# Kernel optimization log

Hardware: AMD Instinct MI355X
Metric: run time of the kernel (lower is better)

Reference implementation:

```python
import jax, jax.numpy as jnp
import numpy as np

N_NODES = 100000
N_EDGES = 1200000
NFEAT = 64
NHID = 64
NCLASS = 16
BN_EPS = 1e-5
L2_EPS = 1e-12


def setup_inputs() -> dict:
    key = jax.random.key(0)
    ks = jax.random.split(key, 8)
    edge_index = jax.random.randint(ks[0], (2, N_EDGES), 0, N_NODES, dtype=jnp.int64)
    x = jax.random.normal(ks[1], (N_NODES, NFEAT), dtype=jnp.float32)
    # SAGEConv params: lin_l (neighbor path, has bias), lin_r (root path, no bias)
    W_l = jax.random.normal(ks[2], (NHID, NFEAT), dtype=jnp.float32) * (1.0 / np.sqrt(NFEAT))
    b_l = jnp.zeros((NHID,), dtype=jnp.float32)
    W_r = jax.random.normal(ks[3], (NHID, NFEAT), dtype=jnp.float32) * (1.0 / np.sqrt(NFEAT))
    # BatchNorm1d affine params
    gamma = jnp.ones((NHID,), dtype=jnp.float32)
    beta = jnp.zeros((NHID,), dtype=jnp.float32)
    # final fc (xavier-ish scale, zero bias per weights_init)
    W_fc = jax.random.normal(ks[4], (NCLASS, NHID), dtype=jnp.float32) * (1.0 / np.sqrt(NHID))
    b_fc = jnp.zeros((NCLASS,), dtype=jnp.float32)
    return {"edge_index": edge_index, "x": x, "W_l": W_l, "b_l": b_l,
            "W_r": W_r, "gamma": gamma, "beta": beta, "W_fc": W_fc, "b_fc": b_fc}


def reference(edge_index, x, W_l, b_l, W_r, gamma, beta, W_fc, b_fc):
    N = x.shape[0]
    src, dst = edge_index[0], edge_index[1]
    # SAGEConv mean aggregation: gather x at source nodes, scatter-mean to dst
    msgs = x[src]                                                  # [E, F]
    sums = jax.ops.segment_sum(msgs, dst, num_segments=N)         # [N, F]
    cnt = jax.ops.segment_sum(jnp.ones((src.shape[0], 1), x.dtype), dst, num_segments=N)
    mean = sums / jnp.maximum(cnt, 1.0)
    # out = lin_l(mean_neighbors) + lin_r(x_root)
    h = mean @ W_l.T + b_l + x @ W_r.T                              # [N, H]
    # normalize=True -> L2 normalize rows (F.normalize semantics)
    h = h / jnp.maximum(jnp.linalg.norm(h, axis=-1, keepdims=True), L2_EPS)
    # transition: ReLU -> BatchNorm1d (training stats) -> Dropout (identity in eval)
    h = jax.nn.relu(h)
    mu = jnp.mean(h, axis=0)
    var = jnp.var(h, axis=0)
    h = (h - mu) / jnp.sqrt(var + BN_EPS) * gamma + beta
    return h @ W_fc.T + b_fc                                        # [N, C]
```

## Files before the change

kernel.cpp:

```cpp
#include <hip/hip_runtime.h>
#include <hip/hip_bf16.h>


typedef __attribute__((ext_vector_type(8))) short short8;
typedef __attribute__((ext_vector_type(4))) float f32x4;

__device__ __forceinline__ unsigned short f2bf(float f) {
    unsigned int u = __builtin_bit_cast(unsigned int, f);
    u += 0x7FFFu + ((u >> 16) & 1u);
    return (unsigned short)(u >> 16);
}
__device__ __forceinline__ float bf2f(unsigned short s) {
    return __builtin_bit_cast(float, ((unsigned int)s) << 16);
}

#define CHUNK 8192

__global__ __launch_bounds__(256) void k_prep(const int* __restrict__ eidx,
                                              int* __restrict__ cnt,
                                              const float4* __restrict__ x4,
                                              ushort4* __restrict__ xbf,
                                              int E, int NB, int NBLK,
                                              int n4, int do_x) {
    __shared__ int lh[256];
    const int tid = threadIdx.x;
    if ((int)blockIdx.x < NBLK) {
        lh[tid] = 0;
        __syncthreads();
        const int base = blockIdx.x * CHUNK;
        for (int i = tid; i < CHUNK; i += 256) {
            int e = base + i;
            if (e < E) atomicAdd(&lh[eidx[E + e] >> 9], 1);
        }
        __syncthreads();
        if (tid < NB) cnt[(size_t)tid * NBLK + blockIdx.x] = lh[tid];
    } else if (do_x) {
        int t = ((int)blockIdx.x - NBLK) * 256 + tid;
        if (t < n4) {
            float4 v = x4[t];
            xbf[t] = make_ushort4(f2bf(v.x), f2bf(v.y), f2bf(v.z), f2bf(v.w));
        }
    }
}

__global__ __launch_bounds__(256) void k_scanbkt(int* __restrict__ cnt,
                                                 int* __restrict__ btot,
                                                 int NBLK) {
    __shared__ int swv[4];
    const int b = blockIdx.x;
    const int t = threadIdx.x;
    int v = (t < NBLK) ? cnt[(size_t)b * NBLK + t] : 0;
    const int lane = t & 63, wid = t >> 6;
    int s = v;
#pragma unroll
    for (int off = 1; off < 64; off <<= 1) {
        int tt = __shfl_up(s, off);
        if (lane >= off) s += tt;
    }
    if (lane == 63) swv[wid] = s;
    __syncthreads();
    if (t == 0) {
        int a = 0;
#pragma unroll
        for (int w = 0; w < 4; ++w) { int tt = swv[w]; swv[w] = a; a += tt; }
    }
    __syncthreads();
    int excl = s - v + swv[wid];
    if (t < NBLK) cnt[(size_t)b * NBLK + t] = excl;
    if (t == 255) btot[b] = swv[3] + s;
}

__global__ __launch_bounds__(256) void k_bscanB(const int* __restrict__ btot,
                                                int* __restrict__ bbase,
                                                int* __restrict__ rowptr,
                                                int NB, int N, int E) {
    __shared__ int swv[4];
    const int t = threadIdx.x;
    int v = (t < NB) ? btot[t] : 0;
    const int lane = t & 63, wid = t >> 6;
    int s = v;
#pragma unroll
    for (int off = 1; off < 64; off <<= 1) {
        int tt = __shfl_up(s, off);
        if (lane >= off) s += tt;
    }
    if (lane == 63) swv[wid] = s;
    __syncthreads();
    if (t == 0) {
        int a = 0;
#pragma unroll
        for (int w = 0; w < 4; ++w) { int tt = swv[w]; swv[w] = a; a += tt; }
    }
    __syncthreads();
    if (t < NB) bbase[t] = s - v + swv[wid];
    if (t == 0) { bbase[NB] = E; rowptr[N] = E; }
}

__global__ __launch_bounds__(256) void k_bscatter(const int* __restrict__ eidx,
                                                  const int* __restrict__ cnt,
                                                  const int* __restrict__ bbase,
                                                  unsigned int* __restrict__ ebuf,
                                                  int E, int NB, int NBLK) {
    __shared__ int cur[256];
    const int tid = threadIdx.x;
    if (tid < NB)
        cur[tid] = bbase[tid] + cnt[(size_t)tid * NBLK + blockIdx.x];
    __syncthreads();
    const int base = blockIdx.x * CHUNK;
    for (int i = tid; i < CHUNK; i += 256) {
        int e = base + i;
        if (e < E) {
            int d = eidx[E + e];
            int s = eidx[e];
            int p = atomicAdd(&cur[d >> 9], 1);
            ebuf[p] = (unsigned int)s | ((unsigned int)(d & 511) << 17);
        }
    }
}

__global__ __launch_bounds__(256) void k_bfinal(const unsigned int* __restrict__ ebuf,
                                                const int* __restrict__ bbase,
                                                int* __restrict__ rowptr,
                                                int* __restrict__ colv, int N) {
    __shared__ int h[512];
    __shared__ int swv[4];
    const int b = blockIdx.x;
    const int tid = threadIdx.x;
    h[2 * tid] = 0;
    h[2 * tid + 1] = 0;
    __syncthreads();
    const int segb = bbase[b], sege = bbase[b + 1];
    for (int i = segb + tid; i < sege; i += 256)
        atomicAdd(&h[ebuf[i] >> 17], 1);
    __syncthreads();
    int a0 = h[2 * tid], a1 = h[2 * tid + 1];
    int ts = a0 + a1;
    const int lane = tid & 63, wid = tid >> 6;
    int s = ts;
#pragma unroll
    for (int off = 1; off < 64; off <<= 1) {
        int tt = __shfl_up(s, off);
        if (lane >= off) s += tt;
    }
    if (lane == 63) swv[wid] = s;
    __syncthreads();
    if (tid == 0) {
        int a = 0;
#pragma unroll
        for (int w = 0; w < 4; ++w) { int tt = swv[w]; swv[w] = a; a += tt; }
    }
    __syncthreads();
    int excl = s - ts + swv[wid];
    h[2 * tid] = excl;
    h[2 * tid + 1] = excl + a0;
    int node = b * 512 + 2 * tid;
    if (node < N) rowptr[node] = segb + excl;
    if (node + 1 < N) rowptr[node + 1] = segb + excl + a0;
    __syncthreads();
    for (int i = segb + tid; i < sege; i += 256) {
        unsigned int u = ebuf[i];
        int p = atomicAdd(&h[u >> 17], 1);
        colv[segb + p] = (int)(u & 0x1FFFFu);
    }
}

__global__ __launch_bounds__(256) void k_gather_bf(
        const uint2* __restrict__ xbf2, const int* __restrict__ rowptr,
        const int* __restrict__ colv, uint2* __restrict__ mh2, int N) {
    int t = blockIdx.x * 256 + threadIdx.x;
    int n = t >> 4;
    int l = t & 15;
    if (n >= N) return;
    int b = rowptr[n], e = rowptr[n + 1];
    float a0 = 0.f, a1 = 0.f, a2 = 0.f, a3 = 0.f;
    int p = b;
    for (; p + 4 <= e; p += 4) {
        int s0 = colv[p], s1 = colv[p + 1], s2 = colv[p + 2], s3 = colv[p + 3];
        uint2 v0 = xbf2[(size_t)s0 * 16 + l];
        uint2 v1 = xbf2[(size_t)s1 * 16 + l];
        uint2 v2 = xbf2[(size_t)s2 * 16 + l];
        uint2 v3 = xbf2[(size_t)s3 * 16 + l];
        a0 += bf2f((unsigned short)(v0.x & 0xFFFF)) + bf2f((unsigned short)(v1.x & 0xFFFF)) +
              bf2f((unsigned short)(v2.x & 0xFFFF)) + bf2f((unsigned short)(v3.x & 0xFFFF));
        a1 += bf2f((unsigned short)(v0.x >> 16)) + bf2f((unsigned short)(v1.x >> 16)) +
              bf2f((unsigned short)(v2.x >> 16)) + bf2f((unsigned short)(v3.x >> 16));
        a2 += bf2f((unsigned short)(v0.y & 0xFFFF)) + bf2f((unsigned short)(v1.y & 0xFFFF)) +
              bf2f((unsigned short)(v2.y & 0xFFFF)) + bf2f((unsigned short)(v3.y & 0xFFFF));
        a3 += bf2f((unsigned short)(v0.y >> 16)) + bf2f((unsigned short)(v1.y >> 16)) +
              bf2f((unsigned short)(v2.y >> 16)) + bf2f((unsigned short)(v3.y >> 16));
    }
    for (; p < e; ++p) {
        int s0 = colv[p];
        uint2 v0 = xbf2[(size_t)s0 * 16 + l];
        a0 += bf2f((unsigned short)(v0.x & 0xFFFF));
        a1 += bf2f((unsigned short)(v0.x >> 16));
        a2 += bf2f((unsigned short)(v0.y & 0xFFFF));
        a3 += bf2f((unsigned short)(v0.y >> 16));
    }
    float inv = 1.0f / fmaxf((float)(e - b), 1.0f);
    uint2 o;
    o.x = (unsigned int)f2bf(a0 * inv) | ((unsigned int)f2bf(a1 * inv) << 16);
    o.y = (unsigned int)f2bf(a2 * inv) | ((unsigned int)f2bf(a3 * inv) << 16);
    mh2[(size_t)n * 16 + l] = o;
}

__global__ __launch_bounds__(256) void k_gather_f32(
        const float4* __restrict__ x4, const int* __restrict__ rowptr,
        const int* __restrict__ colv, ushort4* __restrict__ mh, int N) {
    int t = blockIdx.x * 256 + threadIdx.x;
    int n = t >> 4;
    int l = t & 15;
    if (n >= N) return;
    int b = rowptr[n], e = rowptr[n + 1];
    float ax = 0.f, ay = 0.f, az = 0.f, aw = 0.f;
    int p = b;
    for (; p + 4 <= e; p += 4) {
        int s0 = colv[p], s1 = colv[p + 1], s2 = colv[p + 2], s3 = colv[p + 3];
        float4 v0 = x4[(size_t)s0 * 16 + l];
        float4 v1 = x4[(size_t)s1 * 16 + l];
        float4 v2 = x4[(size_t)s2 * 16 + l];
        float4 v3 = x4[(size_t)s3 * 16 + l];
        ax += (v0.x + v1.x) + (v2.x + v3.x);
        ay += (v0.y + v1.y) + (v2.y + v3.y);
        az += (v0.z + v1.z) + (v2.z + v3.z);
        aw += (v0.w + v1.w) + (v2.w + v3.w);
    }
    for (; p < e; ++p) {
        int s0 = colv[p];
        float4 v0 = x4[(size_t)s0 * 16 + l];
        ax += v0.x; ay += v0.y; az += v0.z; aw += v0.w;
    }
    float inv = 1.0f / fmaxf((float)(e - b), 1.0f);
    mh[(size_t)n * 16 + l] = make_ushort4(f2bf(ax * inv), f2bf(ay * inv),
                                          f2bf(az * inv), f2bf(aw * inv));
}

__global__ __launch_bounds__(256) void k_fused(
        const float* __restrict__ x,
        const unsigned short* __restrict__ xbf, int use_bf,
        const float* __restrict__ Wl, const float* __restrict__ bl,
        const float* __restrict__ Wr,
        unsigned short* __restrict__ mh,
        float* __restrict__ pstats, int N) {
    __shared__ float sRed[4][128];

    const int tid = threadIdx.x;
    const int wid = tid >> 6;
    const int lane = tid & 63;
    const int l15 = lane & 15;
    const int quad = lane >> 4;

    short8 bfrag[4][4];
#pragma unroll
    for (int c = 0; c < 4; ++c) {
#pragma unroll
        for (int f = 0; f < 4; ++f) {
            const int n = f * 16 + l15;
            const float* wsrc = (c < 2)
                ? (Wl + (size_t)n * 64 + c * 32 + quad * 8)
                : (Wr + (size_t)n * 64 + (c - 2) * 32 + quad * 8);
            float4 w0 = *(const float4*)wsrc;
            float4 w1 = *(const float4*)(wsrc + 4);
            union { short8 v; unsigned short u[8]; } pk;
            pk.u[0] = f2bf(w0.x); pk.u[1] = f2bf(w0.y);
            pk.u[2] = f2bf(w0.z); pk.u[3] = f2bf(w0.w);
            pk.u[4] = f2bf(w1.x); pk.u[5] = f2bf(w1.y);
            pk.u[6] = f2bf(w1.z); pk.u[7] = f2bf(w1.w);
            bfrag[c][f] = pk.v;
        }
    }

    float blv[4];
#pragma unroll
    for (int f = 0; f < 4; ++f) blv[f] = bl[f * 16 + l15];

    float psum[4] = {0.f, 0.f, 0.f, 0.f};
    float psq[4] = {0.f, 0.f, 0.f, 0.f};

    for (int t4 = 0; t4 < 4; ++t4) {
        const int tbase = blockIdx.x * 256 + wid * 64 + t4 * 16;
        const int mrow = tbase + l15;
        const int mld = (mrow < N) ? mrow : (N - 1);
        f32x4 acc[4] = {{0.f, 0.f, 0.f, 0.f}, {0.f, 0.f, 0.f, 0.f},
                        {0.f, 0.f, 0.f, 0.f}, {0.f, 0.f, 0.f, 0.f}};
#pragma unroll
        for (int c = 0; c < 2; ++c) {
            short8 a = *(const short8*)(mh + (size_t)mld * 64 + c * 32 + quad * 8);
#pragma unroll
            for (int f = 0; f < 4; ++f)
                acc[f] = __builtin_amdgcn_mfma_f32_16x16x32_bf16(a, bfrag[c][f], acc[f], 0, 0, 0);
        }
        if (use_bf) {
#pragma unroll
            for (int c = 0; c < 2; ++c) {
                short8 a = *(const short8*)(xbf + (size_t)mld * 64 + c * 32 + quad * 8);
#pragma unroll
                for (int f = 0; f < 4; ++f)
                    acc[f] = __builtin_amdgcn_mfma_f32_16x16x32_bf16(a, bfrag[c + 2][f], acc[f], 0, 0, 0);
            }
        } else {
#pragma unroll
            for (int c = 0; c < 2; ++c) {
                const float* xp = x + (size_t)mld * 64 + c * 32 + quad * 8;
                float4 a0 = *(const float4*)xp;
                float4 a1 = *(const float4*)(xp + 4);
                union { short8 v; unsigned short u[8]; } pk;
                pk.u[0] = f2bf(a0.x); pk.u[1] = f2bf(a0.y);
                pk.u[2] = f2bf(a0.z); pk.u[3] = f2bf(a0.w);
                pk.u[4] = f2bf(a1.x); pk.u[5] = f2bf(a1.y);
                pk.u[6] = f2bf(a1.z); pk.u[7] = f2bf(a1.w);
#pragma unroll
                for (int f = 0; f < 4; ++f)
                    acc[f] = __builtin_amdgcn_mfma_f32_16x16x32_bf16(pk.v, bfrag[c + 2][f], acc[f], 0, 0, 0);
            }
        }

#pragma unroll
        for (int reg = 0; reg < 4; ++reg) {
            const int node = tbase + quad * 4 + reg;
            float hv[4];
            float ss = 0.f;
#pragma unroll
            for (int f = 0; f < 4; ++f) {
                hv[f] = acc[f][reg] + blv[f];
                ss += hv[f] * hv[f];
            }
            ss += __shfl_xor(ss, 1);
            ss += __shfl_xor(ss, 2);
            ss += __shfl_xor(ss, 4);
            ss += __shfl_xor(ss, 8);
            float sc = 1.0f / fmaxf(sqrtf(ss), 1e-12f);
            if (node < N) {
#pragma unroll
                for (int f = 0; f < 4; ++f) {
                    float r = fmaxf(hv[f] * sc, 0.f);
                    unsigned short rb = f2bf(r);
                    float e = bf2f(rb);
                    mh[(size_t)node * 64 + f * 16 + l15] = rb;
                    psum[f] += e;
                    psq[f] += e * e;
                }
            }
        }
    }

#pragma unroll
    for (int f = 0; f < 4; ++f) {
        psum[f] += __shfl_xor(psum[f], 16);
        psum[f] += __shfl_xor(psum[f], 32);
        psq[f] += __shfl_xor(psq[f], 16);
        psq[f] += __shfl_xor(psq[f], 32);
    }
    if (lane < 16) {
#pragma unroll
        for (int f = 0; f < 4; ++f) {
            sRed[wid][f * 16 + l15] = psum[f];
            sRed[wid][64 + f * 16 + l15] = psq[f];
        }
    }
    __syncthreads();
    if (tid < 128) {
        float v = sRed[0][tid] + sRed[1][tid] + sRed[2][tid] + sRed[3][tid];
        pstats[(size_t)blockIdx.x * 128 + tid] = v;
    }
}

__global__ __launch_bounds__(64) void k_stats(const float* __restrict__ pstats,
                                              float* __restrict__ stats, int nblk) {
    int col = blockIdx.x;
    int l = threadIdx.x;
    float s = 0.f;
    for (int r = l; r < nblk; r += 64) s += pstats[(size_t)r * 128 + col];
    s += __shfl_xor(s, 1);
    s += __shfl_xor(s, 2);
    s += __shfl_xor(s, 4);
    s += __shfl_xor(s, 8);
    s += __shfl_xor(s, 16);
    s += __shfl_xor(s, 32);
    if (l == 0) stats[col] = s;
}

__global__ __launch_bounds__(256) void k_out(
        const unsigned short* __restrict__ h, const float* __restrict__ stats,
        const float* __restrict__ gamma, const float* __restrict__ beta,
        const float* __restrict__ Wfc, const float* __restrict__ bfc,
        float* __restrict__ out, int N) {
    __shared__ float sWm[64 * 16];
    __shared__ float sShift[64];
    __shared__ float sBase[16];
    const int tid = threadIdx.x;
    const float invN = 1.0f / (float)N;
    if (tid < 64) {
        float mu = stats[tid] * invN;
        float var = stats[64 + tid] * invN - mu * mu;
        float sc = gamma[tid] / sqrtf(var + 1e-5f);
        sShift[tid] = beta[tid] - mu * sc;
#pragma unroll
        for (int c = 0; c < 16; ++c) sWm[tid * 16 + c] = Wfc[c * 64 + tid] * sc;
    }
    __syncthreads();
    if (tid < 16) {
        float b = bfc[tid];
#pragma unroll
        for (int j = 0; j < 64; ++j) b += sShift[j] * Wfc[tid * 64 + j];
        sBase[tid] = b;
    }
    __syncthreads();
    int g = blockIdx.x * 256 + tid;
    int n = g >> 4;
    int c = g & 15;
    if (n >= N) return;
    const ushort4* h4 = (const ushort4*)(h + (size_t)n * 64);
    float acc = sBase[c];
#pragma unroll
    for (int jq = 0; jq < 16; ++jq) {
        ushort4 v = h4[jq];
        acc += bf2f(v.x) * sWm[(jq * 4 + 0) * 16 + c];
        acc += bf2f(v.y) * sWm[(jq * 4 + 1) * 16 + c];
        acc += bf2f(v.z) * sWm[(jq * 4 + 2) * 16 + c];
        acc += bf2f(v.w) * sWm[(jq * 4 + 3) * 16 + c];
    }
    out[(size_t)n * 16 + c] = acc;
}

extern "C" void kernel_launch(void* const* d_in, const int* in_sizes, int n_in,
                              void* d_out, int out_size, void* d_ws, size_t ws_size,
                              hipStream_t stream) {
    const int* eidx = (const int*)d_in[0];
    const float* x = (const float*)d_in[1];
    const float* Wl = (const float*)d_in[2];
    const float* bl = (const float*)d_in[3];
    const float* Wr = (const float*)d_in[4];
    const float* gamma = (const float*)d_in[5];
    const float* beta = (const float*)d_in[6];
    const float* Wfc = (const float*)d_in[7];
    const float* bfc = (const float*)d_in[8];
    float* out = (float*)d_out;

    const int E = in_sizes[0] / 2;
    const int N = in_sizes[1] / 64;
    const int NB = (N + 511) >> 9;
    const int NBLK = (E + CHUNK - 1) / CHUNK;
    const int fb2 = (N + 255) / 256;
    const int n4 = N * 16;

    int* cnt = (int*)d_ws;
    int* btot = cnt + (size_t)NB * NBLK;
    int* bbase = btot + NB;
    int* rowptr = bbase + NB + 1;
    float* pstats = (float*)(rowptr + N + 1);
    float* stats = pstats + (size_t)fb2 * 128;
    int* colv = (int*)(stats + 128);
    unsigned int* ebuf = (unsigned int*)(colv + E);
    unsigned short* mh = (unsigned short*)(ebuf + E);
    unsigned short* xbf = mh + (size_t)N * 64;

    size_t need_bf = (size_t)((char*)(xbf + (size_t)N * 64) - (char*)d_ws);
    const int use_bf = (ws_size >= need_bf) ? 1 : 0;

    int cbl = use_bf ? (n4 + 255) / 256 : 0;
    k_prep<<<NBLK + cbl, 256, 0, stream>>>(eidx, cnt, (const float4*)x,
                                           (ushort4*)xbf, E, NB, NBLK, n4, use_bf);
    k_scanbkt<<<NB, 256, 0, stream>>>(cnt, btot, NBLK);
    k_bscanB<<<1, 256, 0, stream>>>(btot, bbase, rowptr, NB, N, E);
    k_bscatter<<<NBLK, 256, 0, stream>>>(eidx, cnt, bbase, ebuf, E, NB, NBLK);
    k_bfinal<<<NB, 256, 0, stream>>>(ebuf, bbase, rowptr, colv, N);

    int gblocks = (int)(((size_t)N * 16 + 255) / 256);
    if (use_bf) {
        k_gather_bf<<<gblocks, 256, 0, stream>>>((const uint2*)xbf, rowptr, colv,
                                                 (uint2*)mh, N);
    } else {
        k_gather_f32<<<gblocks, 256, 0, stream>>>((const float4*)x, rowptr, colv,
                                                  (ushort4*)mh, N);
    }

    k_fused<<<fb2, 256, 0, stream>>>(x, xbf, use_bf, Wl, bl, Wr, mh, pstats, N);
    k_stats<<<128, 64, 0, stream>>>(pstats, stats, fb2);

    int oblocks = (int)(((size_t)N * 16 + 255) / 256);
    k_out<<<oblocks, 256, 0, stream>>>(mh, stats, gamma, beta, Wfc, bfc, out, N);
}
```

Measured before the change: 212.0 us.

## Merge CSR build and tail stages into cooperative kernels with grid sync

Replaces the five CSR-construction launches (histogram, per-bucket scan, bucket-base scan, scatter, per-bucket final sort) with one cooperative kernel that uses grid.sync between phases and recomputes the small bucket scan redundantly per block. It also fuses the linear/normalize/stats kernel, the stats reduction and the output projection into one cooperative kernel, with each block reducing the partial stats itself. The aim is to remove launch gaps and intermediate kernel boundaries, at the cost of grid-wide barriers and a grid capped by occupancy, so the bf16 cast loop now strides over fewer blocks. Both paths fall back to the old launches when the device does not support cooperative launch or occupancy is insufficient.

```diff
diff --git a/kernel.cpp b/kernel.cpp
--- a/kernel.cpp
+++ b/kernel.cpp
@@ -1,5 +1,8 @@
 #include <hip/hip_runtime.h>
 #include <hip/hip_bf16.h>
+#include <hip/hip_cooperative_groups.h>
+
+namespace cg = cooperative_groups;
 
 
 typedef __attribute__((ext_vector_type(8))) short short8;
@@ -15,6 +18,135 @@
 }
 
 #define CHUNK 8192
+
+__device__ __forceinline__ int exclScan256(int v, int* swv) {
+    const int t = threadIdx.x, lane = t & 63, wid = t >> 6;
+    __syncthreads();
+    int s = v;
+#pragma unroll
+    for (int off = 1; off < 64; off <<= 1) {
+        int tt = __shfl_up(s, off);
+        if (lane >= off) s += tt;
+    }
+    if (lane == 63) swv[wid] = s;
+    __syncthreads();
+    if (t == 0) {
+        int a = 0;
+#pragma unroll
+        for (int w = 0; w < 4; ++w) { int tt = swv[w]; swv[w] = a; a += tt; }
+    }
+    __syncthreads();
+    return s - v + swv[wid];
+}
+
+__global__ __launch_bounds__(256) void k_csr(
+        const int* __restrict__ eidx, int* __restrict__ cnt,
+        int* __restrict__ btot,
+        const float4* __restrict__ x4, ushort4* __restrict__ xbf,
+        unsigned int* __restrict__ ebuf,
+        int* __restrict__ rowptr, int* __restrict__ colv,
+        int E, int N, int NB, int NBLK, int n4, int do_x) {
+    cg::grid_group grid = cg::this_grid();
+    __shared__ int sh[512];
+    __shared__ int sb[257];
+    __shared__ int swv[4];
+    const int tid = threadIdx.x;
+    const int bid = blockIdx.x;
+    const int GD = gridDim.x;
+
+    if (bid < NBLK) {
+        sh[tid] = 0;
+        __syncthreads();
+        const int base = bid * CHUNK;
+        for (int i = tid; i < CHUNK; i += 256) {
+            int e = base + i;
+            if (e < E) atomicAdd(&sh[eidx[E + e] >> 9], 1);
+        }
+        __syncthreads();
+        if (tid < NB) cnt[(size_t)tid * NBLK + bid] = sh[tid];
+    } else if (do_x) {
+        const int ncast = GD - NBLK;
+        for (int i = (bid - NBLK) * 256 + tid; i < n4; i += ncast * 256) {
+            float4 v = x4[i];
+            xbf[i] = make_ushort4(f2bf(v.x), f2bf(v.y), f2bf(v.z), f2bf(v.w));
+        }
+    }
+    __threadfence();
+    grid.sync();
+
+    if (bid < NB) {
+        int v = (tid < NBLK) ? cnt[(size_t)bid * NBLK + tid] : 0;
+        int excl = exclScan256(v, swv);
+        if (tid < NBLK) cnt[(size_t)bid * NBLK + tid] = excl;
+        if (tid == 255) btot[bid] = excl + v;
+    }
+    __threadfence();
+    grid.sync();
+
+    if (bid < NBLK) {
+        int bv = (tid < NB) ? btot[tid] : 0;
+        int bexcl = exclScan256(bv, swv);
+        sh[tid] = (tid < NB) ? (bexcl + cnt[(size_t)tid * NBLK + bid]) : 0;
+        __syncthreads();
+        const int base = bid * CHUNK;
+        for (int i = tid; i < CHUNK; i += 256) {
+            int e = base + i;
+            if (e < E) {
+                int d = eidx[E + e];
+                int s = eidx[e];
+                int p = atomicAdd(&sh[d >> 9], 1);
+                ebuf[p] = (unsigned int)s | ((unsigned int)(d & 511) << 17);
+            }
+        }
+    }
+    __threadfence();
+    grid.sync();
+
+    if (bid < NB) {
+        int bv = (tid < NB) ? btot[tid] : 0;
+        int bexcl = exclScan256(bv, swv);
+        sb[tid] = bexcl;
+        __syncthreads();
+        const int segb = sb[bid];
+        const int sege = segb + btot[bid];
+        sh[2 * tid] = 0;
+        sh[2 * tid + 1] = 0;
+        __syncthreads();
+        for (int i = segb + tid; i < sege; i += 256)
+            atomicAdd(&sh[ebuf[i] >> 17], 1);
+        __syncthreads();
+        int a0 = sh[2 * tid], a1 = sh[2 * tid + 1];
+        int ts = a0 + a1;
+        const int lane = tid & 63, wid = tid >> 6;
+        int s = ts;
+#pragma unroll
+        for (int off = 1; off < 64; off <<= 1) {
+            int tt = __shfl_up(s, off);
+            if (lane >= off) s += tt;
+        }
+        if (lane == 63) swv[wid] = s;
+        __syncthreads();
+        if (tid == 0) {
+            int a = 0;
+#pragma unroll
+            for (int w = 0; w < 4; ++w) { int tt = swv[w]; swv[w] = a; a += tt; }
+        }
+        __syncthreads();
+        int excl = s - ts + swv[wid];
+        sh[2 * tid] = excl;
+        sh[2 * tid + 1] = excl + a0;
+        int node = bid * 512 + 2 * tid;
+        if (node < N) rowptr[node] = segb + excl;
+        if (node + 1 < N) rowptr[node + 1] = segb + excl + a0;
+        __syncthreads();
+        for (int i = segb + tid; i < sege; i += 256) {
+            unsigned int u = ebuf[i];
+            int p = atomicAdd(&sh[u >> 17], 1);
+            colv[segb + p] = (int)(u & 0x1FFFFu);
+        }
+        if (bid == 0 && tid == 0) rowptr[N] = E;
+    }
+}
 
 __global__ __launch_bounds__(256) void k_prep(const int* __restrict__ eidx,
                                               int* __restrict__ cnt,
@@ -50,24 +182,9 @@
     const int b = blockIdx.x;
     const int t = threadIdx.x;
     int v = (t < NBLK) ? cnt[(size_t)b * NBLK + t] : 0;
-    const int lane = t & 63, wid = t >> 6;
-    int s = v;
-#pragma unroll
-    for (int off = 1; off < 64; off <<= 1) {
-        int tt = __shfl_up(s, off);
-        if (lane >= off) s += tt;
-    }
-    if (lane == 63) swv[wid] = s;
-    __syncthreads();
-    if (t == 0) {
-        int a = 0;
-#pragma unroll
-        for (int w = 0; w < 4; ++w) { int tt = swv[w]; swv[w] = a; a += tt; }
-    }
-    __syncthreads();
-    int excl = s - v + swv[wid];
+    int excl = exclScan256(v, swv);
     if (t < NBLK) cnt[(size_t)b * NBLK + t] = excl;
-    if (t == 255) btot[b] = swv[3] + s;
+    if (t == 255) btot[b] = excl + v;
 }
 
 __global__ __launch_bounds__(256) void k_bscanB(const int* __restrict__ btot,
@@ -77,22 +194,8 @@
     __shared__ int swv[4];
     const int t = threadIdx.x;
     int v = (t < NB) ? btot[t] : 0;
-    const int lane = t & 63, wid = t >> 6;
-    int s = v;
-#pragma unroll
-    for (int off = 1; off < 64; off <<= 1) {
-        int tt = __shfl_up(s, off);
-        if (lane >= off) s += tt;
-    }
-    if (lane == 63) swv[wid] = s;
-    __syncthreads();
-    if (t == 0) {
-        int a = 0;
-#pragma unroll
-        for (int w = 0; w < 4; ++w) { int tt = swv[w]; swv[w] = a; a += tt; }
-    }
-    __syncthreads();
-    if (t < NB) bbase[t] = s - v + swv[wid];
+    int excl = exclScan256(v, swv);
+    if (t < NB) bbase[t] = excl;
     if (t == 0) { bbase[NB] = E; rowptr[N] = E; }
 }
 
@@ -235,15 +338,13 @@
                                           f2bf(az * inv), f2bf(aw * inv));
 }
 
-__global__ __launch_bounds__(256) void k_fused(
+__device__ __forceinline__ void fused_body(
         const float* __restrict__ x,
         const unsigned short* __restrict__ xbf, int use_bf,
         const float* __restrict__ Wl, const float* __restrict__ bl,
         const float* __restrict__ Wr,
-        unsigned short* __restrict__ mh,
-        float* __restrict__ pstats, int N) {
-    __shared__ float sRed[4][128];
-
+        unsigned short* __restrict__ mh, float* __restrict__ pstats,
+        int N, float (*sRed)[128]) {
     const int tid = threadIdx.x;
     const int wid = tid >> 6;
     const int lane = tid & 63;
@@ -363,6 +464,88 @@
         float v = sRed[0][tid] + sRed[1][tid] + sRed[2][tid] + sRed[3][tid];
         pstats[(size_t)blockIdx.x * 128 + tid] = v;
     }
+}
+
+__global__ __launch_bounds__(256) void k_tail(
+        const float* __restrict__ x,
+        const unsigned short* __restrict__ xbf, int use_bf,
+        const float* __restrict__ Wl, const float* __restrict__ bl,
+        const float* __restrict__ Wr,
+        unsigned short* __restrict__ mh, float* __restrict__ pstats,
+        const float* __restrict__ gamma, const float* __restrict__ beta,
+        const float* __restrict__ Wfc, const float* __restrict__ bfc,
+        float* __restrict__ out, int N, int fb2) {
+    cg::grid_group grid = cg::this_grid();
+    __shared__ float sRed[4][128];
+    __shared__ float sP[256];
+    __shared__ float sStats[128];
+    __shared__ float sWm[64 * 16];
+    __shared__ float sShift[64];
+    __shared__ float sBase[16];
+    const int tid = threadIdx.x;
+    const int bid = blockIdx.x;
+
+    fused_body(x, xbf, use_bf, Wl, bl, Wr, mh, pstats, N, sRed);
+    __threadfence();
+    grid.sync();
+
+    {
+        const int col = tid & 127, half = tid >> 7;
+        float s = 0.f;
+        for (int r = half; r < fb2; r += 2) s += pstats[(size_t)r * 128 + col];
+        sP[tid] = s;
+        __syncthreads();
+        if (tid < 128) sStats[tid] = sP[tid] + sP[tid + 128];
+        __syncthreads();
+    }
+
+    const float invN = 1.0f / (float)N;
+    if (tid < 64) {
+        float mu = sStats[tid] * invN;
+        float var = sStats[64 + tid] * invN - mu * mu;
+        float sc = gamma[tid] / sqrtf(var + 1e-5f);
+        sShift[tid] = beta[tid] - mu * sc;
+#pragma unroll
+        for (int c = 0; c < 16; ++c) sWm[tid * 16 + c] = Wfc[c * 64 + tid] * sc;
+    }
+    __syncthreads();
+    if (tid < 16) {
+        float b = bfc[tid];
+#pragma unroll
+        for (int j = 0; j < 64; ++j) b += sShift[j] * Wfc[tid * 64 + j];
+        sBase[tid] = b;
+    }
+    __syncthreads();
+#pragma unroll
+    for (int it = 0; it < 16; ++it) {
+        int g = it * 256 + tid;
+        int nl = g >> 4;
+        int c = g & 15;
+        int n = bid * 256 + nl;
+        if (n < N) {
+            const ushort4* h4 = (const ushort4*)(mh + (size_t)n * 64);
+            float acc = sBase[c];
+#pragma unroll
+            for (int jq = 0; jq < 16; ++jq) {
+                ushort4 v = h4[jq];
+                acc += bf2f(v.x) * sWm[(jq * 4 + 0) * 16 + c];
+                acc += bf2f(v.y) * sWm[(jq * 4 + 1) * 16 + c];
+                acc += bf2f(v.z) * sWm[(jq * 4 + 2) * 16 + c];
+                acc += bf2f(v.w) * sWm[(jq * 4 + 3) * 16 + c];
+            }
+            out[(size_t)n * 16 + c] = acc;
+        }
+    }
+}
+
+__global__ __launch_bounds__(256) void k_fused(
+        const float* __restrict__ x,
+        const unsigned short* __restrict__ xbf, int use_bf,
+        const float* __restrict__ Wl, const float* __restrict__ bl,
+        const float* __restrict__ Wr,
+        unsigned short* __restrict__ mh, float* __restrict__ pstats, int N) {
+    __shared__ float sRed[4][128];
+    fused_body(x, xbf, use_bf, Wl, bl, Wr, mh, pstats, N, sRed);
 }
 
 __global__ __launch_bounds__(64) void k_stats(const float* __restrict__ pstats,
@@ -452,19 +635,53 @@
     float* stats = pstats + (size_t)fb2 * 128;
     int* colv = (int*)(stats + 128);
     unsigned int* ebuf = (unsigned int*)(colv + E);
-    unsigned short* mh = (unsigned short*)(ebuf + E);
+    unsigned short* mh = (unsigned short*)(((uintptr_t)(ebuf + E) + 15) & ~(uintptr_t)15);
     unsigned short* xbf = mh + (size_t)N * 64;
 
     size_t need_bf = (size_t)((char*)(xbf + (size_t)N * 64) - (char*)d_ws);
     const int use_bf = (ws_size >= need_bf) ? 1 : 0;
 
-    int cbl = use_bf ? (n4 + 255) / 256 : 0;
-    k_prep<<<NBLK + cbl, 256, 0, stream>>>(eidx, cnt, (const float4*)x,
-                                           (ushort4*)xbf, E, NB, NBLK, n4, use_bf);
-    k_scanbkt<<<NB, 256, 0, stream>>>(cnt, btot, NBLK);
-    k_bscanB<<<1, 256, 0, stream>>>(btot, bbase, rowptr, NB, N, E);
-    k_bscatter<<<NBLK, 256, 0, stream>>>(eidx, cnt, bbase, ebuf, E, NB, NBLK);
-    k_bfinal<<<NB, 256, 0, stream>>>(ebuf, bbase, rowptr, colv, N);
+    static int g_init = 0;
+    static int g_numCU = 0, g_coopDev = 0, g_mCsr = 0, g_mTail = 0;
+    if (!g_init) {
+        int dev = 0;
+        hipGetDevice(&dev);
+        hipDeviceProp_t prop{};
+        hipGetDeviceProperties(&prop, dev);
+        g_numCU = prop.multiProcessorCount;
+        g_coopDev = prop.cooperativeLaunch;
+        hipOccupancyMaxActiveBlocksPerMultiprocessor(&g_mCsr, reinterpret_cast<const void*>(k_csr), 256, 0);
+        hipOccupancyMaxActiveBlocksPerMultiprocessor(&g_mTail, reinterpret_cast<const void*>(k_tail), 256, 0);
+        g_init = 1;
+    }
+
+    const int maxNBx = (NB > NBLK) ? NB : NBLK;
+    int gridCsr = g_mCsr * g_numCU;
+    if (gridCsr > 1024) gridCsr = 1024;
+    const bool coop_csr = g_coopDev && (gridCsr >= maxNBx + 64);
+    const bool coop_tail = g_coopDev && (g_mTail * g_numCU >= fb2);
+
+    if (coop_csr) {
+        const int* eidx_ = eidx;
+        int* cnt_ = cnt; int* btot_ = btot;
+        const float4* x4_ = (const float4*)x;
+        ushort4* xbf4_ = (ushort4*)xbf;
+        unsigned int* ebuf_ = ebuf;
+        int* rowptr_ = rowptr; int* colv_ = colv;
+        int E_ = E, N_ = N, NB_ = NB, NBLK_ = NBLK, n4_ = n4, ub_ = use_bf;
+        void* args[] = {&eidx_, &cnt_, &btot_, &x4_, &xbf4_, &ebuf_,
+                        &rowptr_, &colv_, &E_, &N_, &NB_, &NBLK_, &n4_, &ub_};
+        hipLaunchCooperativeKernel(reinterpret_cast<const void*>(k_csr),
+                                   dim3(gridCsr), dim3(256), args, 0, stream);
+    } else {
+        int cbl = use_bf ? (n4 + 255) / 256 : 0;
+        k_prep<<<NBLK + cbl, 256, 0, stream>>>(eidx, cnt, (const float4*)x,
+                                               (ushort4*)xbf, E, NB, NBLK, n4, use_bf);
+        k_scanbkt<<<NB, 256, 0, stream>>>(cnt, btot, NBLK);
+        k_bscanB<<<1, 256, 0, stream>>>(btot, bbase, rowptr, NB, N, E);
+        k_bscatter<<<NBLK, 256, 0, stream>>>(eidx, cnt, bbase, ebuf, E, NB, NBLK);
+        k_bfinal<<<NB, 256, 0, stream>>>(ebuf, bbase, rowptr, colv, N);
+    }
 
     int gblocks = (int)(((size_t)N * 16 + 255) / 256);
     if (use_bf) {
@@ -475,9 +692,24 @@
                                                   (ushort4*)mh, N);
     }
 
-    k_fused<<<fb2, 256, 0, stream>>>(x, xbf, use_bf, Wl, bl, Wr, mh, pstats, N);
-    k_stats<<<128, 64, 0, stream>>>(pstats, stats, fb2);
-
-    int oblocks = (int)(((size_t)N * 16 + 255) / 256);
-    k_out<<<oblocks, 256, 0, stream>>>(mh, stats, gamma, beta, Wfc, bfc, out, N);
-}
+    if (coop_tail) {
+        const float* x_ = x;
+        const unsigned short* xbf_ = xbf;
+        int ub_ = use_bf;
+        const float* Wl_ = Wl; const float* bl_ = bl; const float* Wr_ = Wr;
+        unsigned short* mh_ = mh; float* pstats_ = pstats;
+        const float* g_ = gamma; const float* b_ = beta;
+        const float* Wfc_ = Wfc; const float* bfc_ = bfc;
+        float* out_ = out;
+        int N_ = N, fb2_ = fb2;
+        void* args[] = {&x_, &xbf_, &ub_, &Wl_, &bl_, &Wr_, &mh_, &pstats_,
+                        &g_, &b_, &Wfc_, &bfc_, &out_, &N_, &fb2_};
+        hipLaunchCooperativeKernel(reinterpret_cast<const void*>(k_tail),
+                                   dim3(fb2), dim3(256), args, 0, stream);
+    } else {
+        k_fused<<<fb2, 256, 0, stream>>>(x, xbf, use_bf, Wl, bl, Wr, mh, pstats, N);
+        k_stats<<<128, 64, 0, stream>>>(pstats, stats, fb2);
+        int oblocks = (int)(((size_t)N * 16 + 255) / 256);
+        k_out<<<oblocks, 256, 0, stream>>>(mh, stats, gamma, beta, Wfc, bfc, out, N);
+    }
+}
```

Result: slower. 800.5 us (+277.6%).

## Remove two small kernels by redundant bucket scans and last-block stats reduction

Applied to the files above, without the earlier changes.

Drops the single-block bucket-base scan kernel: each scatter and final block now redoes the 196-entry exclusive scan over bucket totals itself. The separate column-stats kernel is also removed. k_fused now uses a global atomic counter so that the last finishing block reduces the per-block partial sums. This cuts two launches and their serialization gaps, at the cost of redundant scans per block and a serial tail reduction done by one block.

```diff
diff --git a/kernel.cpp b/kernel.cpp
--- a/kernel.cpp
+++ b/kernel.cpp
@@ -16,15 +16,37 @@
 
 #define CHUNK 8192
 
+__device__ __forceinline__ int exclScan256(int v, int* swv) {
+    const int t = threadIdx.x, lane = t & 63, wid = t >> 6;
+    __syncthreads();
+    int s = v;
+#pragma unroll
+    for (int off = 1; off < 64; off <<= 1) {
+        int tt = __shfl_up(s, off);
+        if (lane >= off) s += tt;
+    }
+    if (lane == 63) swv[wid] = s;
+    __syncthreads();
+    if (t == 0) {
+        int a = 0;
+#pragma unroll
+        for (int w = 0; w < 4; ++w) { int tt = swv[w]; swv[w] = a; a += tt; }
+    }
+    __syncthreads();
+    return s - v + swv[wid];
+}
+
 __global__ __launch_bounds__(256) void k_prep(const int* __restrict__ eidx,
                                               int* __restrict__ cnt,
                                               const float4* __restrict__ x4,
                                               ushort4* __restrict__ xbf,
+                                              int* __restrict__ done,
                                               int E, int NB, int NBLK,
                                               int n4, int do_x) {
     __shared__ int lh[256];
     const int tid = threadIdx.x;
     if ((int)blockIdx.x < NBLK) {
+        if (blockIdx.x == 0 && tid == 0) *done = 0;
         lh[tid] = 0;
         __syncthreads();
         const int base = blockIdx.x * CHUNK;
@@ -50,61 +72,23 @@
     const int b = blockIdx.x;
     const int t = threadIdx.x;
     int v = (t < NBLK) ? cnt[(size_t)b * NBLK + t] : 0;
-    const int lane = t & 63, wid = t >> 6;
-    int s = v;
-#pragma unroll
-    for (int off = 1; off < 64; off <<= 1) {
-        int tt = __shfl_up(s, off);
-        if (lane >= off) s += tt;
-    }
-    if (lane == 63) swv[wid] = s;
-    __syncthreads();
-    if (t == 0) {
-        int a = 0;
-#pragma unroll
-        for (int w = 0; w < 4; ++w) { int tt = swv[w]; swv[w] = a; a += tt; }
-    }
-    __syncthreads();
-    int excl = s - v + swv[wid];
+    int excl = exclScan256(v, swv);
     if (t < NBLK) cnt[(size_t)b * NBLK + t] = excl;
-    if (t == 255) btot[b] = swv[3] + s;
-}
-
-__global__ __launch_bounds__(256) void k_bscanB(const int* __restrict__ btot,
-                                                int* __restrict__ bbase,
-                                                int* __restrict__ rowptr,
-                                                int NB, int N, int E) {
-    __shared__ int swv[4];
-    const int t = threadIdx.x;
-    int v = (t < NB) ? btot[t] : 0;
-    const int lane = t & 63, wid = t >> 6;
-    int s = v;
-#pragma unroll
-    for (int off = 1; off < 64; off <<= 1) {
-        int tt = __shfl_up(s, off);
-        if (lane >= off) s += tt;
-    }
-    if (lane == 63) swv[wid] = s;
-    __syncthreads();
-    if (t == 0) {
-        int a = 0;
-#pragma unroll
-        for (int w = 0; w < 4; ++w) { int tt = swv[w]; swv[w] = a; a += tt; }
-    }
-    __syncthreads();
-    if (t < NB) bbase[t] = s - v + swv[wid];
-    if (t == 0) { bbase[NB] = E; rowptr[N] = E; }
+    if (t == 255) btot[b] = excl + v;
 }
 
 __global__ __launch_bounds__(256) void k_bscatter(const int* __restrict__ eidx,
                                                   const int* __restrict__ cnt,
-                                                  const int* __restrict__ bbase,
+                                                  const int* __restrict__ btot,
                                                   unsigned int* __restrict__ ebuf,
                                                   int E, int NB, int NBLK) {
     __shared__ int cur[256];
+    __shared__ int swv[4];
     const int tid = threadIdx.x;
+    int bv = (tid < NB) ? btot[tid] : 0;
+    int bexcl = exclScan256(bv, swv);
     if (tid < NB)
-        cur[tid] = bbase[tid] + cnt[(size_t)tid * NBLK + blockIdx.x];
+        cur[tid] = bexcl + cnt[(size_t)tid * NBLK + blockIdx.x];
     __syncthreads();
     const int base = blockIdx.x * CHUNK;
     for (int i = tid; i < CHUNK; i += 256) {
@@ -119,17 +103,22 @@
 }
 
 __global__ __launch_bounds__(256) void k_bfinal(const unsigned int* __restrict__ ebuf,
-                                                const int* __restrict__ bbase,
+                                                const int* __restrict__ btot,
                                                 int* __restrict__ rowptr,
-                                                int* __restrict__ colv, int N) {
+                                                int* __restrict__ colv,
+                                                int N, int NB, int E) {
     __shared__ int h[512];
     __shared__ int swv[4];
+    __shared__ int sseg[2];
     const int b = blockIdx.x;
     const int tid = threadIdx.x;
+    int bv = (tid < NB) ? btot[tid] : 0;
+    int bexcl = exclScan256(bv, swv);
+    if (tid == b) { sseg[0] = bexcl; sseg[1] = bexcl + bv; }
     h[2 * tid] = 0;
     h[2 * tid + 1] = 0;
     __syncthreads();
-    const int segb = bbase[b], sege = bbase[b + 1];
+    const int segb = sseg[0], sege = sseg[1];
     for (int i = segb + tid; i < sege; i += 256)
         atomicAdd(&h[ebuf[i] >> 17], 1);
     __syncthreads();
@@ -162,6 +151,7 @@
         int p = atomicAdd(&h[u >> 17], 1);
         colv[segb + p] = (int)(u & 0x1FFFFu);
     }
+    if (b == 0 && tid == 0) rowptr[N] = E;
 }
 
 __global__ __launch_bounds__(256) void k_gather_bf(
@@ -241,8 +231,11 @@
         const float* __restrict__ Wl, const float* __restrict__ bl,
         const float* __restrict__ Wr,
         unsigned short* __restrict__ mh,
-        float* __restrict__ pstats, int N) {
+        float* __restrict__ pstats, float* __restrict__ stats,
+        int* __restrict__ done, int fb2, int N) {
     __shared__ float sRed[4][128];
+    __shared__ float sP[256];
+    __shared__ int isLast;
 
     const int tid = threadIdx.x;
     const int wid = tid >> 6;
@@ -363,21 +356,22 @@
         float v = sRed[0][tid] + sRed[1][tid] + sRed[2][tid] + sRed[3][tid];
         pstats[(size_t)blockIdx.x * 128 + tid] = v;
     }
-}
-
-__global__ __launch_bounds__(64) void k_stats(const float* __restrict__ pstats,
-                                              float* __restrict__ stats, int nblk) {
-    int col = blockIdx.x;
-    int l = threadIdx.x;
-    float s = 0.f;
-    for (int r = l; r < nblk; r += 64) s += pstats[(size_t)r * 128 + col];
-    s += __shfl_xor(s, 1);
-    s += __shfl_xor(s, 2);
-    s += __shfl_xor(s, 4);
-    s += __shfl_xor(s, 8);
-    s += __shfl_xor(s, 16);
-    s += __shfl_xor(s, 32);
-    if (l == 0) stats[col] = s;
+
+    if (tid == 0) {
+        __threadfence();
+        int v = atomicAdd(done, 1);
+        isLast = (v == fb2 - 1);
+    }
+    __syncthreads();
+    if (isLast) {
+        __threadfence();
+        const int col = tid & 127, half = tid >> 7;
+        float s = 0.f;
+        for (int r = half; r < fb2; r += 2) s += pstats[(size_t)r * 128 + col];
+        sP[tid] = s;
+        __syncthreads();
+        if (tid < 128) stats[tid] = sP[tid] + sP[tid + 128];
+    }
 }
 
 __global__ __launch_bounds__(256) void k_out(
@@ -446,13 +440,13 @@
 
     int* cnt = (int*)d_ws;
     int* btot = cnt + (size_t)NB * NBLK;
-    int* bbase = btot + NB;
-    int* rowptr = bbase + NB + 1;
+    int* done = btot + NB;
+    int* rowptr = done + NB + 1;
     float* pstats = (float*)(rowptr + N + 1);
     float* stats = pstats + (size_t)fb2 * 128;
     int* colv = (int*)(stats + 128);
     unsigned int* ebuf = (unsigned int*)(colv + E);
-    unsigned short* mh = (unsigned short*)(ebuf + E);
+    unsigned short* mh = (unsigned short*)(((uintptr_t)(ebuf + E) + 15) & ~(uintptr_t)15);
     unsigned short* xbf = mh + (size_t)N * 64;
 
     size_t need_bf = (size_t)((char*)(xbf + (size_t)N * 64) - (char*)d_ws);
@@ -460,11 +454,11 @@
 
     int cbl = use_bf ? (n4 + 255) / 256 : 0;
     k_prep<<<NBLK + cbl, 256, 0, stream>>>(eidx, cnt, (const float4*)x,
-                                           (ushort4*)xbf, E, NB, NBLK, n4, use_bf);
+                                           (ushort4*)xbf, done, E, NB, NBLK,
+                                           n4, use_bf);
     k_scanbkt<<<NB, 256, 0, stream>>>(cnt, btot, NBLK);
-    k_bscanB<<<1, 256, 0, stream>>>(btot, bbase, rowptr, NB, N, E);
-    k_bscatter<<<NBLK, 256, 0, stream>>>(eidx, cnt, bbase, ebuf, E, NB, NBLK);
-    k_bfinal<<<NB, 256, 0, stream>>>(ebuf, bbase, rowptr, colv, N);
+    k_bscatter<<<NBLK, 256, 0, stream>>>(eidx, cnt, btot, ebuf, E, NB, NBLK);
+    k_bfinal<<<NB, 256, 0, stream>>>(ebuf, btot, rowptr, colv, N, NB, E);
 
     int gblocks = (int)(((size_t)N * 16 + 255) / 256);
     if (use_bf) {
@@ -475,8 +469,8 @@
                                                   (ushort4*)mh, N);
     }
 
-    k_fused<<<fb2, 256, 0, stream>>>(x, xbf, use_bf, Wl, bl, Wr, mh, pstats, N);
-    k_stats<<<128, 64, 0, stream>>>(pstats, stats, fb2);
+    k_fused<<<fb2, 256, 0, stream>>>(x, xbf, use_bf, Wl, bl, Wr, mh,
+                                     pstats, stats, done, fb2, N);
 
     int oblocks = (int)(((size_t)N * 16 + 255) / 256);
     k_out<<<oblocks, 256, 0, stream>>>(mh, stats, gamma, beta, Wfc, bfc, out, N);
```

Measured after the change: 269.7 us. 27.2% more time.

## Fold bucket-count scans into scatter and final kernels, removing two launches

Applied to the files above, without the earlier changes.

Drops the separate per-bucket scan and bucket-base scan kernels. Each block of k_bscatter and k_bfinal now redundantly reads the full block-major count table (NBLK x 256) and does a block-wide exclusive scan to work out its own offsets. This removes two small, serial launches from the CSR build chain. In exchange every block does extra redundant global reads and a scan, and the mh pointer is now aligned to 16 bytes.

```diff
diff --git a/kernel.cpp b/kernel.cpp
--- a/kernel.cpp
+++ b/kernel.cpp
@@ -15,6 +15,26 @@
 }
 
 #define CHUNK 8192
+
+__device__ __forceinline__ int exclScan256(int v, int* swv) {
+    const int t = threadIdx.x, lane = t & 63, wid = t >> 6;
+    __syncthreads();
+    int s = v;
+#pragma unroll
+    for (int off = 1; off < 64; off <<= 1) {
+        int tt = __shfl_up(s, off);
+        if (lane >= off) s += tt;
+    }
+    if (lane == 63) swv[wid] = s;
+    __syncthreads();
+    if (t == 0) {
+        int a = 0;
+#pragma unroll
+        for (int w = 0; w < 4; ++w) { int tt = swv[w]; swv[w] = a; a += tt; }
+    }
+    __syncthreads();
+    return s - v + swv[wid];
+}
 
 __global__ __launch_bounds__(256) void k_prep(const int* __restrict__ eidx,
                                               int* __restrict__ cnt,
@@ -33,7 +53,7 @@
             if (e < E) atomicAdd(&lh[eidx[E + e] >> 9], 1);
         }
         __syncthreads();
-        if (tid < NB) cnt[(size_t)tid * NBLK + blockIdx.x] = lh[tid];
+        cnt[(size_t)blockIdx.x * 256 + tid] = lh[tid];
     } else if (do_x) {
         int t = ((int)blockIdx.x - NBLK) * 256 + tid;
         if (t < n4) {
@@ -43,70 +63,24 @@
     }
 }
 
-__global__ __launch_bounds__(256) void k_scanbkt(int* __restrict__ cnt,
-                                                 int* __restrict__ btot,
-                                                 int NBLK) {
-    __shared__ int swv[4];
-    const int b = blockIdx.x;
-    const int t = threadIdx.x;
-    int v = (t < NBLK) ? cnt[(size_t)b * NBLK + t] : 0;
-    const int lane = t & 63, wid = t >> 6;
-    int s = v;
-#pragma unroll
-    for (int off = 1; off < 64; off <<= 1) {
-        int tt = __shfl_up(s, off);
-        if (lane >= off) s += tt;
-    }
-    if (lane == 63) swv[wid] = s;
-    __syncthreads();
-    if (t == 0) {
-        int a = 0;
-#pragma unroll
-        for (int w = 0; w < 4; ++w) { int tt = swv[w]; swv[w] = a; a += tt; }
-    }
-    __syncthreads();
-    int excl = s - v + swv[wid];
-    if (t < NBLK) cnt[(size_t)b * NBLK + t] = excl;
-    if (t == 255) btot[b] = swv[3] + s;
-}
-
-__global__ __launch_bounds__(256) void k_bscanB(const int* __restrict__ btot,
-                                                int* __restrict__ bbase,
-                                                int* __restrict__ rowptr,
-                                                int NB, int N, int E) {
-    __shared__ int swv[4];
-    const int t = threadIdx.x;
-    int v = (t < NB) ? btot[t] : 0;
-    const int lane = t & 63, wid = t >> 6;
-    int s = v;
-#pragma unroll
-    for (int off = 1; off < 64; off <<= 1) {
-        int tt = __shfl_up(s, off);
-        if (lane >= off) s += tt;
-    }
-    if (lane == 63) swv[wid] = s;
-    __syncthreads();
-    if (t == 0) {
-        int a = 0;
-#pragma unroll
-        for (int w = 0; w < 4; ++w) { int tt = swv[w]; swv[w] = a; a += tt; }
-    }
-    __syncthreads();
-    if (t < NB) bbase[t] = s - v + swv[wid];
-    if (t == 0) { bbase[NB] = E; rowptr[N] = E; }
-}
-
 __global__ __launch_bounds__(256) void k_bscatter(const int* __restrict__ eidx,
                                                   const int* __restrict__ cnt,
-                                                  const int* __restrict__ bbase,
                                                   unsigned int* __restrict__ ebuf,
                                                   int E, int NB, int NBLK) {
     __shared__ int cur[256];
+    __shared__ int swv[4];
     const int tid = threadIdx.x;
-    if (tid < NB)
-        cur[tid] = bbase[tid] + cnt[(size_t)tid * NBLK + blockIdx.x];
-    __syncthreads();
-    const int base = blockIdx.x * CHUNK;
+    const int b = blockIdx.x;
+    int pre = 0, tot = 0;
+    for (int c = 0; c < NBLK; ++c) {
+        int v = cnt[(size_t)c * 256 + tid];
+        tot += v;
+        if (c < b) pre += v;
+    }
+    int bexcl = exclScan256(tot, swv);
+    cur[tid] = bexcl + pre;
+    __syncthreads();
+    const int base = b * CHUNK;
     for (int i = tid; i < CHUNK; i += 256) {
         int e = base + i;
         if (e < E) {
@@ -119,17 +93,24 @@
 }
 
 __global__ __launch_bounds__(256) void k_bfinal(const unsigned int* __restrict__ ebuf,
-                                                const int* __restrict__ bbase,
+                                                const int* __restrict__ cnt,
                                                 int* __restrict__ rowptr,
-                                                int* __restrict__ colv, int N) {
+                                                int* __restrict__ colv,
+                                                int N, int NB, int NBLK, int E) {
     __shared__ int h[512];
     __shared__ int swv[4];
+    __shared__ int sseg[2];
     const int b = blockIdx.x;
     const int tid = threadIdx.x;
+    int tot = 0;
+    for (int c = 0; c < NBLK; ++c)
+        tot += cnt[(size_t)c * 256 + tid];
+    int bexcl = exclScan256(tot, swv);
+    if (tid == b) { sseg[0] = bexcl; sseg[1] = bexcl + tot; }
     h[2 * tid] = 0;
     h[2 * tid + 1] = 0;
     __syncthreads();
-    const int segb = bbase[b], sege = bbase[b + 1];
+    const int segb = sseg[0], sege = sseg[1];
     for (int i = segb + tid; i < sege; i += 256)
         atomicAdd(&h[ebuf[i] >> 17], 1);
     __syncthreads();
@@ -162,6 +143,7 @@
         int p = atomicAdd(&h[u >> 17], 1);
         colv[segb + p] = (int)(u & 0x1FFFFu);
     }
+    if (b == 0 && tid == 0) rowptr[N] = E;
 }
 
 __global__ __launch_bounds__(256) void k_gather_bf(
@@ -445,14 +427,12 @@
     const int n4 = N * 16;
 
     int* cnt = (int*)d_ws;
-    int* btot = cnt + (size_t)NB * NBLK;
-    int* bbase = btot + NB;
-    int* rowptr = bbase + NB + 1;
+    int* rowptr = cnt + (size_t)NBLK * 256;
     float* pstats = (float*)(rowptr + N + 1);
     float* stats = pstats + (size_t)fb2 * 128;
     int* colv = (int*)(stats + 128);
     unsigned int* ebuf = (unsigned int*)(colv + E);
-    unsigned short* mh = (unsigned short*)(ebuf + E);
+    unsigned short* mh = (unsigned short*)(((uintptr_t)(ebuf + E) + 15) & ~(uintptr_t)15);
     unsigned short* xbf = mh + (size_t)N * 64;
 
     size_t need_bf = (size_t)((char*)(xbf + (size_t)N * 64) - (char*)d_ws);
@@ -461,10 +441,8 @@
     int cbl = use_bf ? (n4 + 255) / 256 : 0;
     k_prep<<<NBLK + cbl, 256, 0, stream>>>(eidx, cnt, (const float4*)x,
                                            (ushort4*)xbf, E, NB, NBLK, n4, use_bf);
-    k_scanbkt<<<NB, 256, 0, stream>>>(cnt, btot, NBLK);
-    k_bscanB<<<1, 256, 0, stream>>>(btot, bbase, rowptr, NB, N, E);
-    k_bscatter<<<NBLK, 256, 0, stream>>>(eidx, cnt, bbase, ebuf, E, NB, NBLK);
-    k_bfinal<<<NB, 256, 0, stream>>>(ebuf, bbase, rowptr, colv, N);
+    k_bscatter<<<NBLK, 256, 0, stream>>>(eidx, cnt, ebuf, E, NB, NBLK);
+    k_bfinal<<<NB, 256, 0, stream>>>(ebuf, cnt, rowptr, colv, N, NB, NBLK, E);
 
     int gblocks = (int)(((size_t)N * 16 + 255) / 256);
     if (use_bf) {
```

Result: slower. 240.7 us (+13.5%).
